# Performance work log

Measured on AMD Instinct MI355X. Metric: run time of the kernel, lower is better.

Reference implementation:

```python
import jax, jax.numpy as jnp
import numpy as np

EPS = 1e-05


def layer_norm(x, scale):
    # Faithful to source bug: returns scale * x_norm + scale (shift param unused)
    mean = jnp.mean(x, axis=-1, keepdims=True)
    var = jnp.var(x, axis=-1, keepdims=True)  # unbiased=False
    x_norm = (x - mean) / jnp.sqrt(var + EPS)
    return scale * x_norm + scale


def mhsa(x, wq, wk, wv, wo, bo, n_heads):
    b, t, d = x.shape
    hd = d // n_heads
    # torch Linear: y = x @ W.T (no qkv bias)
    q = (x @ wq.T).reshape(b, t, n_heads, hd).transpose(0, 2, 1, 3)  # bhtd
    k = (x @ wk.T).reshape(b, t, n_heads, hd).transpose(0, 2, 1, 3)
    v = (x @ wv.T).reshape(b, t, n_heads, hd).transpose(0, 2, 1, 3)
    scores = jnp.einsum('bhqd,bhkd->bhqk', q, k)
    causal = jnp.triu(jnp.ones((t, t), dtype=bool), k=1)
    scores = jnp.where(causal, -jnp.inf, scores)
    attn = jax.nn.softmax(scores / np.sqrt(hd).astype(np.float32), axis=-1)
    ctx = jnp.einsum('bhqk,bhkd->bhqd', attn, v)
    ctx = ctx.transpose(0, 2, 1, 3).reshape(b, t, d)
    return ctx @ wo.T + bo


def setup_inputs() -> dict:
    key = jax.random.key(0)
    ks = jax.random.split(key, 6)
    B, T, D = 2, 2048, 1024
    return {
        'x': jax.random.normal(ks[0], (B, T, D), dtype=jnp.float32),
        'wq': jax.random.normal(ks[1], (D, D), dtype=jnp.float32) * 0.02,
        'wk': jax.random.normal(ks[2], (D, D), dtype=jnp.float32) * 0.02,
        'wv': jax.random.normal(ks[3], (D, D), dtype=jnp.float32) * 0.02,
        'wo': jax.random.normal(ks[4], (D, D), dtype=jnp.float32) * 0.02,
        'bo': jnp.zeros((D,), dtype=jnp.float32),
        'ln1_scale': jnp.ones((D,), dtype=jnp.float32),
        'ln2_scale': jnp.ones((D,), dtype=jnp.float32),
    }


def reference(x, wq, wk, wv, wo, bo, ln1_scale, ln2_scale):
    n_heads = 16
    # Block 1: norm1 -> attn -> (+residual); dropout is identity in eval mode
    h = x + mhsa(layer_norm(x, ln1_scale), wq, wk, wv, wo, bo, n_heads)
    # Block 2: source calls self.attn (same weights) again, not self.ff
    out = h + mhsa(layer_norm(h, ln2_scale), wq, wk, wv, wo, bo, n_heads)
    return out
```

## Files before the change

### kernel.cpp

```cpp
#include <hip/hip_runtime.h>
#include <hip/hip_bf16.h>
#include <math.h>

#define Dm 1024
#define Tm 2048
#define Bm 2
#define Hm 16
#define HDm 64
#define Rm (Bm*Tm)
#define QKS 2048

typedef __attribute__((ext_vector_type(8))) short sh8;
typedef __attribute__((ext_vector_type(4))) float f32x4;

#define AS1(p) ((const __attribute__((address_space(1))) void*)(p))
#define AS3(p) ((__attribute__((address_space(3))) void*)(p))

__device__ __forceinline__ short f2bs(float f) {
    union { float f; unsigned u; } v; v.f = f;
    unsigned r = v.u + 0x7FFFu + ((v.u >> 16) & 1u);
    return (short)(r >> 16);
}

__global__ __launch_bounds__(256) void convert_w(const float* __restrict__ wq,
                                                 const float* __restrict__ wk,
                                                 const float* __restrict__ wv,
                                                 const float* __restrict__ wo,
                                                 short* __restrict__ wqkv,
                                                 short* __restrict__ wob) {
    int idx = (blockIdx.x * 256 + threadIdx.x) * 4;
    const int M1 = 1 << 20;
    const float* src; short* dst; int off;
    if (idx < M1)           { src = wq; dst = wqkv;          off = idx; }
    else if (idx < 2*M1)    { src = wk; dst = wqkv + M1;     off = idx - M1; }
    else if (idx < 3*M1)    { src = wv; dst = wqkv + 2*M1;   off = idx - 2*M1; }
    else                    { src = wo; dst = wob;           off = idx - 3*M1; }
    float4 v = *(const float4*)(src + off);
    short4 o;
    o.x = f2bs(v.x); o.y = f2bs(v.y); o.z = f2bs(v.z); o.w = f2bs(v.w);
    *(short4*)(dst + off) = o;
}

__global__ __launch_bounds__(256) void ln_kernel(const float* __restrict__ x,
                                                 const float* __restrict__ scale,
                                                 short* __restrict__ out) {
    int row = blockIdx.x;
    int t = threadIdx.x;
    const float4* xr = (const float4*)(x + (size_t)row * Dm);
    float4 v = xr[t];
    float s  = v.x + v.y + v.z + v.w;
    float ss = v.x*v.x + v.y*v.y + v.z*v.z + v.w*v.w;
    #pragma unroll
    for (int off = 32; off; off >>= 1) {
        s  += __shfl_xor(s, off);
        ss += __shfl_xor(ss, off);
    }
    __shared__ float red[8];
    int wave = t >> 6, lane = t & 63;
    if (lane == 0) { red[wave*2] = s; red[wave*2+1] = ss; }
    __syncthreads();
    s  = red[0] + red[2] + red[4] + red[6];
    ss = red[1] + red[3] + red[5] + red[7];
    float mean = s * (1.0f / Dm);
    float var  = ss * (1.0f / Dm) - mean * mean;
    float rstd = 1.0f / sqrtf(var + 1e-5f);
    float4 sc = ((const float4*)scale)[t];
    short4 o;
    o.x = f2bs(sc.x * ((v.x - mean) * rstd) + sc.x);
    o.y = f2bs(sc.y * ((v.y - mean) * rstd) + sc.y);
    o.z = f2bs(sc.z * ((v.z - mean) * rstd) + sc.z);
    o.w = f2bs(sc.w * ((v.w - mean) * rstd) + sc.w);
    ((short4*)(out + (size_t)row * Dm))[t] = o;
}

template<int BN, int MODE>
__global__ __launch_bounds__(256) void gemm_mfma(const short* __restrict__ A,
                                                 const short* __restrict__ B,
                                                 const float* __restrict__ bias,
                                                 const float* __restrict__ res,
                                                 void* __restrict__ Cv,
                                                 short* __restrict__ Vt,
                                                 int M, int N, int K) {
    __shared__ short As[128*32];
    __shared__ short Bs[BN*32];
    __shared__ short Tb[(MODE==1) ? 4*16*68 : 4];
    const int NJ = BN / 32;
    int t = threadIdx.x;
    int lane = t & 63, w = t >> 6;
    int l = lane & 15, quad = lane >> 4;
    int wm = (w & 1) * 64, wn = (w >> 1) * (BN/2);
    int m0 = blockIdx.y * 128, n0 = blockIdx.x * BN;

    f32x4 acc[4][NJ];
    #pragma unroll
    for (int i = 0; i < 4; i++)
        #pragma unroll
        for (int j = 0; j < NJ; j++)
            acc[i][j] = (f32x4){0.f,0.f,0.f,0.f};

    for (int k0 = 0; k0 < K; k0 += 32) {
        __syncthreads();
        #pragma unroll
        for (int p = 0; p < 2; p++) {
            int off = p*4096 + t*16;
            int row = off >> 6;
            int c = ((off >> 4) & 3) ^ (row & 3);
            const short* ga = A + (size_t)(m0 + row) * K + k0 + c*8;
            __builtin_amdgcn_global_load_lds(AS1(ga), AS3((char*)As + off), 16, 0, 0);
        }
        #pragma unroll
        for (int p = 0; p < BN/64; p++) {
            int off = p*4096 + t*16;
            int row = off >> 6;
            int c = ((off >> 4) & 3) ^ (row & 3);
            const short* gb = B + (size_t)(n0 + row) * K + k0 + c*8;
            __builtin_amdgcn_global_load_lds(AS1(gb), AS3((char*)Bs + off), 16, 0, 0);
        }
        __syncthreads();
        sh8 af[4], bf[NJ];
        #pragma unroll
        for (int i = 0; i < 4; i++) {
            int m = wm + i*16 + l;
            af[i] = *(const sh8*)((const char*)As + m*64 + ((quad ^ (m & 3)) * 16));
        }
        #pragma unroll
        for (int j = 0; j < NJ; j++) {
            int n = wn + j*16 + l;
            bf[j] = *(const sh8*)((const char*)Bs + n*64 + ((quad ^ (n & 3)) * 16));
        }
        #pragma unroll
        for (int i = 0; i < 4; i++)
            #pragma unroll
            for (int j = 0; j < NJ; j++)
                acc[i][j] = __builtin_amdgcn_mfma_f32_16x16x32_bf16(af[i], bf[j], acc[i][j], 0, 0, 0);
    }
    if (MODE == 0) {
        #pragma unroll
        for (int i = 0; i < 4; i++)
            #pragma unroll
            for (int j = 0; j < NJ; j++)
                #pragma unroll
                for (int r = 0; r < 4; r++) {
                    int m = m0 + wm + i*16 + quad*4 + r;
                    int n = n0 + wn + j*16 + l;
                    float vv = acc[i][j][r] + bias[n] + res[(size_t)m * N + n];
                    ((float*)Cv)[(size_t)m * N + n] = vv;
                }
    } else {
        if (n0 < 2048) {
            #pragma unroll
            for (int i = 0; i < 4; i++)
                #pragma unroll
                for (int j = 0; j < NJ; j++)
                    #pragma unroll
                    for (int r = 0; r < 4; r++) {
                        int m = m0 + wm + i*16 + quad*4 + r;
                        int n = n0 + wn + j*16 + l;
                        ((short*)Cv)[(size_t)m * QKS + n] = f2bs(acc[i][j][r]);
                    }
        } else {
            int bq = m0 >> 11;
            int key0 = (m0 & 2047) + wm;
            int h = (n0 + wn - 2048) >> 6;
            short* vout = Vt + ((size_t)(bq*Hm + h) * HDm) * Tm + key0;
            #pragma unroll
            for (int j = 0; j < NJ; j++) {
                #pragma unroll
                for (int i = 0; i < 4; i++) {
                    short4 o;
                    o.x = f2bs(acc[i][j][0]); o.y = f2bs(acc[i][j][1]);
                    o.z = f2bs(acc[i][j][2]); o.w = f2bs(acc[i][j][3]);
                    *(short4*)&Tb[w*(16*68) + l*68 + i*16 + quad*4] = o;
                }
                #pragma unroll
                for (int st = 0; st < 2; st++) {
                    int rr = st*8 + (lane >> 3);
                    int cc = lane & 7;
                    sh8 vv = *(const sh8*)&Tb[w*(16*68) + rr*68 + cc*8];
                    *(sh8*)(vout + (size_t)(j*16 + rr) * Tm + cc*8) = vv;
                }
            }
        }
    }
}

#define KP 72

__device__ __forceinline__ void stage_kv(const short* kp0, const short* vh,
                                         int kbase, short* Kd, short* Vd, int t) {
    #pragma unroll
    for (int p = 0; p < 2; p++) {
        int off = p*4096 + t*16;
        int row = off >> 7;
        int c = ((off >> 4) & 7) ^ (row & 7);
        const short* gk = kp0 + (size_t)(kbase + row) * QKS + c*8;
        __builtin_amdgcn_global_load_lds(AS1(gk), AS3((char*)Kd + off), 16, 0, 0);
        const short* gv = vh + (size_t)row * Tm + kbase + c*8;
        __builtin_amdgcn_global_load_lds(AS1(gv), AS3((char*)Vd + off), 16, 0, 0);
    }
}

__global__ __launch_bounds__(256) void attn_mfma(const short* __restrict__ qk,
                                                 const short* __restrict__ vtg,
                                                 short* __restrict__ ctx) {
    __shared__ short Kl[2][64*64];
    __shared__ short Vl[2][64*64];
    __shared__ short Pl[4][16*KP];
    int t = threadIdx.x;
    int lane = t & 63, w = t >> 6;
    int l = lane & 15, quad = lane >> 4;
    int pair = blockIdx.x;
    int bh = blockIdx.y;
    int b = bh >> 4, h = bh & 15;
    size_t rbase = (size_t)b * Tm;
    const short* qp0 = qk + rbase * QKS + h*HDm;
    const short* kp0 = qp0 + Dm;
    const short* vh  = vtg + ((size_t)bh * HDm) * Tm;

    int cur = 0;
    stage_kv(kp0, vh, 0, Kl[0], Vl[0], t);
    __syncthreads();

    for (int ph = 0; ph < 2; ph++) {
        int qt = ph ? (31 - pair) : pair;
        int qtbase = qt * 64;

        sh8 qf0, qf1;
        {
            const short* qp = qp0 + (size_t)(qtbase + w*16 + l) * QKS + quad*8;
            qf0 = *(const sh8*)qp;
            qf1 = *(const sh8*)(qp + 32);
        }
        f32x4 O[4] = {{0,0,0,0},{0,0,0,0},{0,0,0,0},{0,0,0,0}};
        float ps[4] = {0.f, 0.f, 0.f, 0.f};

        for (int kc = 0; kc <= qt; kc++) {
            int kbase = kc * 64;
            bool last = (ph == 1) && (kc == qt);
            if (!last) {
                int nb = (kc < qt) ? kbase + 64 : 0;
                stage_kv(kp0, vh, nb, Kl[cur^1], Vl[cur^1], t);
            }

            f32x4 S[4];
            #pragma unroll
            for (int kt = 0; kt < 4; kt++) {
                const f32x4 z = {0.f,0.f,0.f,0.f};
                int key = kt*16 + l;
                const char* kb = (const char*)Kl[cur] + key*128;
                int sw = key & 7;
                sh8 k0 = *(const sh8*)(kb + ((quad ^ sw) * 16));
                sh8 k1 = *(const sh8*)(kb + (((4 + quad) ^ sw) * 16));
                f32x4 s = __builtin_amdgcn_mfma_f32_16x16x32_bf16(k0, qf0, z, 0, 0, 0);
                s = __builtin_amdgcn_mfma_f32_16x16x32_bf16(k1, qf1, s, 0, 0, 0);
                S[kt] = s;
            }
            bool needmask = (kbase + 63 > qtbase + w*16);
            int qrow = qtbase + w*16 + l;
            #pragma unroll
            for (int kt = 0; kt < 4; kt++) {
                float p[4];
                if (needmask) {
                    #pragma unroll
                    for (int r = 0; r < 4; r++) {
                        int key = kbase + kt*16 + quad*4 + r;
                        p[r] = (key > qrow) ? 0.f : __expf(S[kt][r] * 0.125f);
                    }
                } else {
                    #pragma unroll
                    for (int r = 0; r < 4; r++)
                        p[r] = __expf(S[kt][r] * 0.125f);
                }
                ps[kt] += (p[0] + p[1]) + (p[2] + p[3]);
                __hip_bfloat162 pa = __float22bfloat162_rn({p[0], p[1]});
                __hip_bfloat162 pb = __float22bfloat162_rn({p[2], p[3]});
                union { __hip_bfloat162 hh[2]; short4 s4; } u;
                u.hh[0] = pa; u.hh[1] = pb;
                *(short4*)&Pl[w][l*KP + kt*16 + quad*4] = u.s4;
            }
            sh8 p0 = *(const sh8*)&Pl[w][l*KP + quad*8];
            sh8 p1 = *(const sh8*)&Pl[w][l*KP + 32 + quad*8];
            #pragma unroll
            for (int dt = 0; dt < 4; dt++) {
                int d = dt*16 + l;
                const char* vb = (const char*)Vl[cur] + d*128;
                int sw = d & 7;
                sh8 v0 = *(const sh8*)(vb + ((quad ^ sw) * 16));
                sh8 v1 = *(const sh8*)(vb + (((4 + quad) ^ sw) * 16));
                O[dt] = __builtin_amdgcn_mfma_f32_16x16x32_bf16(p0, v0, O[dt], 0, 0, 0);
                O[dt] = __builtin_amdgcn_mfma_f32_16x16x32_bf16(p1, v1, O[dt], 0, 0, 0);
            }
            __syncthreads();
            cur ^= 1;
        }

        float psum = (ps[0] + ps[1]) + (ps[2] + ps[3]);
        psum += __shfl_xor(psum, 16);
        psum += __shfl_xor(psum, 32);
        #pragma unroll
        for (int r = 0; r < 4; r++) {
            int src = (lane & 48) | (((lane >> 4) << 2) + r);
            float inv = 1.0f / __shfl(psum, src);
            int row = qtbase + w*16 + quad*4 + r;
            #pragma unroll
            for (int dt = 0; dt < 4; dt++)
                ctx[(rbase + row) * Dm + h*HDm + dt*16 + l] = f2bs(O[dt][r] * inv);
        }
    }
}

extern "C" void kernel_launch(void* const* d_in, const int* in_sizes, int n_in,
                              void* d_out, int out_size, void* d_ws, size_t ws_size,
                              hipStream_t stream) {
    const float* x   = (const float*)d_in[0];
    const float* wq  = (const float*)d_in[1];
    const float* wk  = (const float*)d_in[2];
    const float* wv  = (const float*)d_in[3];
    const float* wo  = (const float*)d_in[4];
    const float* bo  = (const float*)d_in[5];
    const float* ln1 = (const float*)d_in[6];
    const float* ln2 = (const float*)d_in[7];
    float* out = (float*)d_out;

    short* lnb  = (short*)d_ws;
    short* ctxb = lnb  + (size_t)Rm*Dm;
    short* qk   = ctxb + (size_t)Rm*Dm;
    short* vtg  = qk   + (size_t)Rm*QKS;
    short* wqkv = vtg  + (size_t)Bm*Hm*HDm*Tm;
    short* wob  = wqkv + (size_t)3*Dm*Dm;

    dim3 qgrid(3072/128, Rm/128);
    dim3 pgrid(Dm/64,    Rm/128);
    dim3 agrid(16, Bm*Hm);

    convert_w<<<4096, 256, 0, stream>>>(wq, wk, wv, wo, wqkv, wob);

    ln_kernel<<<Rm, 256, 0, stream>>>(x, ln1, lnb);
    gemm_mfma<128, 1><<<qgrid, 256, 0, stream>>>(lnb, wqkv, nullptr, nullptr, qk, vtg, Rm, 3072, Dm);
    attn_mfma<<<agrid, 256, 0, stream>>>(qk, vtg, ctxb);
    gemm_mfma<64, 0><<<pgrid, 256, 0, stream>>>(ctxb, wob, bo, x, out, nullptr, Rm, Dm, Dm);

    ln_kernel<<<Rm, 256, 0, stream>>>(out, ln2, lnb);
    gemm_mfma<128, 1><<<qgrid, 256, 0, stream>>>(lnb, wqkv, nullptr, nullptr, qk, vtg, Rm, 3072, Dm);
    attn_mfma<<<agrid, 256, 0, stream>>>(qk, vtg, ctxb);
    gemm_mfma<64, 0><<<pgrid, 256, 0, stream>>>(ctxb, wob, bo, out, out, nullptr, Rm, Dm, Dm);
}
```

Before: 320.6 us.

## Split paired causal query tiles into separate blocks and swizzle P tile

Each attention block now processes a single 64-row query tile instead of a balanced pair, doubling the grid and ordering tiles so heavy and light ones interleave during dispatch. The P staging buffer in shared memory drops its padding and uses an XOR swizzle to avoid bank conflicts. This aims for more concurrent blocks and shorter per-block latency. The trade-off is a less even workload per block and repeated K/V staging across the split tiles.

```diff
diff --git a/kernel.cpp b/kernel.cpp
--- a/kernel.cpp
+++ b/kernel.cpp
@@ -184,8 +184,6 @@
     }
 }
 
-#define KP 72
-
 __device__ __forceinline__ void stage_kv(const short* kp0, const short* vh,
                                          int kbase, short* Kd, short* Vd, int t) {
     #pragma unroll
@@ -205,107 +203,105 @@
                                                  short* __restrict__ ctx) {
     __shared__ short Kl[2][64*64];
     __shared__ short Vl[2][64*64];
-    __shared__ short Pl[4][16*KP];
+    __shared__ short Pl[4][16*64];
     int t = threadIdx.x;
     int lane = t & 63, w = t >> 6;
     int l = lane & 15, quad = lane >> 4;
-    int pair = blockIdx.x;
-    int bh = blockIdx.y;
+    int bh = blockIdx.x;
+    int xi = blockIdx.y;
+    int cc0 = xi & 7, kk0 = xi >> 3;
+    int qt = (kk0 == 0) ? cc0 : (kk0 == 1) ? (15 - cc0)
+           : (kk0 == 2) ? (16 + cc0) : (31 - cc0);
     int b = bh >> 4, h = bh & 15;
     size_t rbase = (size_t)b * Tm;
     const short* qp0 = qk + rbase * QKS + h*HDm;
     const short* kp0 = qp0 + Dm;
     const short* vh  = vtg + ((size_t)bh * HDm) * Tm;
+    int qtbase = qt * 64;
+
+    sh8 qf0, qf1;
+    {
+        const short* qp = qp0 + (size_t)(qtbase + w*16 + l) * QKS + quad*8;
+        qf0 = *(const sh8*)qp;
+        qf1 = *(const sh8*)(qp + 32);
+    }
+    f32x4 O[4] = {{0,0,0,0},{0,0,0,0},{0,0,0,0},{0,0,0,0}};
+    float ps[4] = {0.f, 0.f, 0.f, 0.f};
 
     int cur = 0;
     stage_kv(kp0, vh, 0, Kl[0], Vl[0], t);
     __syncthreads();
 
-    for (int ph = 0; ph < 2; ph++) {
-        int qt = ph ? (31 - pair) : pair;
-        int qtbase = qt * 64;
-
-        sh8 qf0, qf1;
-        {
-            const short* qp = qp0 + (size_t)(qtbase + w*16 + l) * QKS + quad*8;
-            qf0 = *(const sh8*)qp;
-            qf1 = *(const sh8*)(qp + 32);
-        }
-        f32x4 O[4] = {{0,0,0,0},{0,0,0,0},{0,0,0,0},{0,0,0,0}};
-        float ps[4] = {0.f, 0.f, 0.f, 0.f};
-
-        for (int kc = 0; kc <= qt; kc++) {
-            int kbase = kc * 64;
-            bool last = (ph == 1) && (kc == qt);
-            if (!last) {
-                int nb = (kc < qt) ? kbase + 64 : 0;
-                stage_kv(kp0, vh, nb, Kl[cur^1], Vl[cur^1], t);
+    int swl = l & 7;
+    for (int kc = 0; kc <= qt; kc++) {
+        int kbase = kc * 64;
+        if (kc < qt)
+            stage_kv(kp0, vh, kbase + 64, Kl[cur^1], Vl[cur^1], t);
+
+        f32x4 S[4];
+        #pragma unroll
+        for (int kt = 0; kt < 4; kt++) {
+            const f32x4 z = {0.f,0.f,0.f,0.f};
+            int key = kt*16 + l;
+            const char* kb = (const char*)Kl[cur] + key*128;
+            int sw = key & 7;
+            sh8 k0 = *(const sh8*)(kb + ((quad ^ sw) * 16));
+            sh8 k1 = *(const sh8*)(kb + (((4 + quad) ^ sw) * 16));
+            f32x4 s = __builtin_amdgcn_mfma_f32_16x16x32_bf16(k0, qf0, z, 0, 0, 0);
+            s = __builtin_amdgcn_mfma_f32_16x16x32_bf16(k1, qf1, s, 0, 0, 0);
+            S[kt] = s;
+        }
+        bool needmask = (kbase + 63 > qtbase + w*16);
+        int qrow = qtbase + w*16 + l;
+        #pragma unroll
+        for (int kt = 0; kt < 4; kt++) {
+            float p[4];
+            if (needmask) {
+                #pragma unroll
+                for (int r = 0; r < 4; r++) {
+                    int key = kbase + kt*16 + quad*4 + r;
+                    p[r] = (key > qrow) ? 0.f : __expf(S[kt][r] * 0.125f);
+                }
+            } else {
+                #pragma unroll
+                for (int r = 0; r < 4; r++)
+                    p[r] = __expf(S[kt][r] * 0.125f);
             }
-
-            f32x4 S[4];
-            #pragma unroll
-            for (int kt = 0; kt < 4; kt++) {
-                const f32x4 z = {0.f,0.f,0.f,0.f};
-                int key = kt*16 + l;
-                const char* kb = (const char*)Kl[cur] + key*128;
-                int sw = key & 7;
-                sh8 k0 = *(const sh8*)(kb + ((quad ^ sw) * 16));
-                sh8 k1 = *(const sh8*)(kb + (((4 + quad) ^ sw) * 16));
-                f32x4 s = __builtin_amdgcn_mfma_f32_16x16x32_bf16(k0, qf0, z, 0, 0, 0);
-                s = __builtin_amdgcn_mfma_f32_16x16x32_bf16(k1, qf1, s, 0, 0, 0);
-                S[kt] = s;
-            }
-            bool needmask = (kbase + 63 > qtbase + w*16);
-            int qrow = qtbase + w*16 + l;
-            #pragma unroll
-            for (int kt = 0; kt < 4; kt++) {
-                float p[4];
-                if (needmask) {
-                    #pragma unroll
-                    for (int r = 0; r < 4; r++) {
-                        int key = kbase + kt*16 + quad*4 + r;
-                        p[r] = (key > qrow) ? 0.f : __expf(S[kt][r] * 0.125f);
-                    }
-                } else {
-                    #pragma unroll
-                    for (int r = 0; r < 4; r++)
-                        p[r] = __expf(S[kt][r] * 0.125f);
-                }
-                ps[kt] += (p[0] + p[1]) + (p[2] + p[3]);
-                __hip_bfloat162 pa = __float22bfloat162_rn({p[0], p[1]});
-                __hip_bfloat162 pb = __float22bfloat162_rn({p[2], p[3]});
-                union { __hip_bfloat162 hh[2]; short4 s4; } u;
-                u.hh[0] = pa; u.hh[1] = pb;
-                *(short4*)&Pl[w][l*KP + kt*16 + quad*4] = u.s4;
-            }
-            sh8 p0 = *(const sh8*)&Pl[w][l*KP + quad*8];
-            sh8 p1 = *(const sh8*)&Pl[w][l*KP + 32 + quad*8];
-            #pragma unroll
-            for (int dt = 0; dt < 4; dt++) {
-                int d = dt*16 + l;
-                const char* vb = (const char*)Vl[cur] + d*128;
-                int sw = d & 7;
-                sh8 v0 = *(const sh8*)(vb + ((quad ^ sw) * 16));
-                sh8 v1 = *(const sh8*)(vb + (((4 + quad) ^ sw) * 16));
-                O[dt] = __builtin_amdgcn_mfma_f32_16x16x32_bf16(p0, v0, O[dt], 0, 0, 0);
-                O[dt] = __builtin_amdgcn_mfma_f32_16x16x32_bf16(p1, v1, O[dt], 0, 0, 0);
-            }
-            __syncthreads();
-            cur ^= 1;
-        }
-
-        float psum = (ps[0] + ps[1]) + (ps[2] + ps[3]);
-        psum += __shfl_xor(psum, 16);
-        psum += __shfl_xor(psum, 32);
-        #pragma unroll
-        for (int r = 0; r < 4; r++) {
-            int src = (lane & 48) | (((lane >> 4) << 2) + r);
-            float inv = 1.0f / __shfl(psum, src);
-            int row = qtbase + w*16 + quad*4 + r;
-            #pragma unroll
-            for (int dt = 0; dt < 4; dt++)
-                ctx[(rbase + row) * Dm + h*HDm + dt*16 + l] = f2bs(O[dt][r] * inv);
-        }
+            ps[kt] += (p[0] + p[1]) + (p[2] + p[3]);
+            __hip_bfloat162 pa = __float22bfloat162_rn({p[0], p[1]});
+            __hip_bfloat162 pb = __float22bfloat162_rn({p[2], p[3]});
+            union { __hip_bfloat162 hh[2]; short4 s4; } u;
+            u.hh[0] = pa; u.hh[1] = pb;
+            int g = (kt*2 + (quad >> 1)) ^ swl;
+            *(short4*)&Pl[w][l*64 + g*8 + (quad & 1)*4] = u.s4;
+        }
+        sh8 p0 = *(const sh8*)&Pl[w][l*64 + ((quad ^ swl) * 8)];
+        sh8 p1 = *(const sh8*)&Pl[w][l*64 + (((4 + quad) ^ swl) * 8)];
+        #pragma unroll
+        for (int dt = 0; dt < 4; dt++) {
+            int d = dt*16 + l;
+            const char* vb = (const char*)Vl[cur] + d*128;
+            int sw = d & 7;
+            sh8 v0 = *(const sh8*)(vb + ((quad ^ sw) * 16));
+            sh8 v1 = *(const sh8*)(vb + (((4 + quad) ^ sw) * 16));
+            O[dt] = __builtin_amdgcn_mfma_f32_16x16x32_bf16(p0, v0, O[dt], 0, 0, 0);
+            O[dt] = __builtin_amdgcn_mfma_f32_16x16x32_bf16(p1, v1, O[dt], 0, 0, 0);
+        }
+        __syncthreads();
+        cur ^= 1;
+    }
+
+    float psum = (ps[0] + ps[1]) + (ps[2] + ps[3]);
+    psum += __shfl_xor(psum, 16);
+    psum += __shfl_xor(psum, 32);
+    #pragma unroll
+    for (int r = 0; r < 4; r++) {
+        int src = (lane & 48) | (((lane >> 4) << 2) + r);
+        float inv = 1.0f / __shfl(psum, src);
+        int row = qtbase + w*16 + quad*4 + r;
+        #pragma unroll
+        for (int dt = 0; dt < 4; dt++)
+            ctx[(rbase + row) * Dm + h*HDm + dt*16 + l] = f2bs(O[dt][r] * inv);
     }
 }
 
@@ -331,7 +327,7 @@
 
     dim3 qgrid(3072/128, Rm/128);
     dim3 pgrid(Dm/64,    Rm/128);
-    dim3 agrid(16, Bm*Hm);
+    dim3 agrid(32, 32);
 
     convert_w<<<4096, 256, 0, stream>>>(wq, wk, wv, wo, wqkv, wob);
 
```

Result: faster. 303.8 us (-5.2%).
